# Optimization experiments

Hardware: AMD Instinct MI355X
Metric: run time of the kernel (lower is better)

Reference implementation:

```python
import jax, jax.numpy as jnp
import numpy as np

MIN_DELAY = 60
MAX_DELAY = 420
TAU = 0.0          # module's self.tau (min magnitude for resonant_activation)
TEMPERATURE = 1.0  # forward() default gumbel-softmax temperature


def setup_inputs() -> dict:
    key = jax.random.key(0)
    k1, k2, k3, k4 = jax.random.split(key, 4)
    B, T = 128, 8192
    excitation = jax.random.normal(k1, (B, 1, T), dtype=jnp.float32)
    u = jax.random.uniform(k2, (MAX_DELAY - MIN_DELAY,), dtype=jnp.float32,
                           minval=1e-6, maxval=1.0 - 1e-6)
    gumbel_noise = -jnp.log(-jnp.log(u))  # standard Gumbel samples
    delay_param = jax.random.normal(k3, (MAX_DELAY - MIN_DELAY,), dtype=jnp.float32)
    feedback_gain = jnp.ones((1,), dtype=jnp.float32)
    reflection_coeffs = jax.random.normal(k4, (2,), dtype=jnp.float32)
    return {"excitation": excitation, "gumbel_noise": gumbel_noise,
            "delay_param": delay_param, "feedback_gain": feedback_gain,
            "reflection_coeffs": reflection_coeffs}


def _resonant_activation(x, min_magnitude):
    sign = jnp.sign(x)
    magnitude = jnp.abs(jnp.tanh(x))
    return sign * (min_magnitude + (1.0 - min_magnitude) * magnitude)


def _build_coeffs(gumbel_noise, delay_param, feedback_gain, reflection_coeffs):
    # gumbel_softmax(tau=TEMPERATURE, hard=True) with straight-through estimator
    logits = (delay_param + gumbel_noise) / TEMPERATURE
    soft = jax.nn.softmax(logits)
    hard = jax.nn.one_hot(jnp.argmax(soft), soft.shape[0], dtype=soft.dtype)
    one_hot = jax.lax.stop_gradient(hard - soft) + soft
    shifted = jnp.roll(one_hot, 1)
    # low_pass_bias=False -> tanh, then resonant_activation (applies tanh again, as in source)
    rc = jnp.tanh(reflection_coeffs)
    k1 = _resonant_activation(rc[0], TAU)
    k2 = _resonant_activation(rc[1], TAU)
    a1 = k1 * (1.0 - k2)
    a2 = jnp.clip(k2, -0.999, 0.999)
    a1_bound = 0.999 - jnp.abs(a2)
    a1 = jnp.clip(a1, -a1_bound, a1_bound)
    g = jax.nn.sigmoid(feedback_gain[0]) ** 0.45
    a1 = a1 * g
    a2 = a2 * g
    tail = one_hot * a1 + shifted * a2               # [max_delay - min_delay]
    coeffs = jnp.concatenate([jnp.zeros((MIN_DELAY,), tail.dtype), tail])  # [max_delay]
    return coeffs


def _sample_wise_lpc(x, coeffs):
    # All-pole IIR: y[t] = x[t] - sum_{i=0}^{D-1} coeffs[i] * y[t-1-i]
    B, T = x.shape
    D = coeffs.shape[0]
    buf0 = jnp.zeros((B, D), x.dtype)  # buf[:, i] = y[t-1-i]

    def step(buf, x_t):
        y_t = x_t - buf @ coeffs                              # [B]
        buf = jnp.concatenate([y_t[:, None], buf[:, :-1]], 1)  # shift delay line
        return buf, y_t

    _, ys = jax.lax.scan(step, buf0, x.T)  # ys: [T, B]
    return ys.T


def reference(excitation, gumbel_noise, delay_param, feedback_gain, reflection_coeffs):
    coeffs = _build_coeffs(gumbel_noise, delay_param, feedback_gain, reflection_coeffs)
    x = excitation[:, 0, :]                 # [B, T]
    y = _sample_wise_lpc(x, coeffs)         # [B, T]
    return y[:, None, :]                    # [B, 1, T]
```

## Files before the change

kernel.cpp:

```cpp
#include <hip/hip_runtime.h>
#include <cmath>

#define T_LEN 8192
#define B_ROWS 128
#define ND 360
#define MIN_DELAY_C 60
#define BLOCK 512

__global__ __launch_bounds__(BLOCK) void ks_resonator_kernel(
    const float* __restrict__ excitation,
    const float* __restrict__ gumbel,
    const float* __restrict__ delay_param,
    const float* __restrict__ feedback_gain,
    const float* __restrict__ refl,
    float* __restrict__ out)
{
    __shared__ float y[T_LEN];
    __shared__ float red_v[BLOCK];
    __shared__ int   red_i[BLOCK];
    __shared__ float s_a1, s_a2;
    __shared__ int   s_lagA, s_lagB;

    const int tid = threadIdx.x;
    const int row = blockIdx.x;

    float v = -INFINITY; int idx = 0;
    if (tid < ND) { v = delay_param[tid] + gumbel[tid]; idx = tid; }
    red_v[tid] = v; red_i[tid] = idx;
    __syncthreads();
    for (int off = BLOCK / 2; off > 0; off >>= 1) {
        if (tid < off) {
            float v2 = red_v[tid + off]; int i2 = red_i[tid + off];
            float v1 = red_v[tid];       int i1 = red_i[tid];
            if (v2 > v1 || (v2 == v1 && i2 < i1)) { red_v[tid] = v2; red_i[tid] = i2; }
        }
        __syncthreads();
    }

    if (tid == 0) {
        int p = red_i[0];
        float k1 = tanhf(tanhf(refl[0]));
        float k2 = tanhf(tanhf(refl[1]));
        float a1 = k1 * (1.0f - k2);
        float a2 = fminf(fmaxf(k2, -0.999f), 0.999f);
        float bound = 0.999f - fabsf(a2);
        a1 = fminf(fmaxf(a1, -bound), bound);
        float fg = feedback_gain[0];
        float g = powf(1.0f / (1.0f + expf(-fg)), 0.45f);
        a1 *= g; a2 *= g;
        int p2 = (p + 1) % ND;
        s_a1 = a1; s_a2 = a2;
        s_lagA = MIN_DELAY_C + p + 1;
        s_lagB = MIN_DELAY_C + p2 + 1;
    }
    __syncthreads();

    const float a1 = s_a1, a2 = s_a2;
    const int lagA = s_lagA, lagB = s_lagB;
    const int C = (lagA < lagB) ? lagA : lagB;

    const float* x = excitation + (size_t)row * T_LEN;
    for (int i = tid; i < T_LEN; i += BLOCK) y[i] = x[i];
    __syncthreads();

    for (int pos = 0; pos < T_LEN; pos += C) {
        int end = pos + C; if (end > T_LEN) end = T_LEN;
        for (int j = pos + tid; j < end; j += BLOCK) {
            float ya = (j >= lagA) ? y[j - lagA] : 0.0f;
            float yb = (j >= lagB) ? y[j - lagB] : 0.0f;
            y[j] = y[j] - a1 * ya - a2 * yb;
        }
        __syncthreads();
    }

    float* o = out + (size_t)row * T_LEN;
    for (int i = tid; i < T_LEN; i += BLOCK) o[i] = y[i];
}

extern "C" void kernel_launch(void* const* d_in, const int* in_sizes, int n_in,
                              void* d_out, int out_size, void* d_ws, size_t ws_size,
                              hipStream_t stream) {
    const float* excitation    = (const float*)d_in[0];
    const float* gumbel        = (const float*)d_in[1];
    const float* delay_param   = (const float*)d_in[2];
    const float* feedback_gain = (const float*)d_in[3];
    const float* refl          = (const float*)d_in[4];
    float* out = (float*)d_out;

    ks_resonator_kernel<<<B_ROWS, BLOCK, 0, stream>>>(
        excitation, gumbel, delay_param, feedback_gain, refl, out);
}
```

Before: 73.14 us.

## Run delay-line recurrence in a single wavefront without block barriers

Replaces the block-wide chunked IIR loop, which needed a __syncthreads per chunk, with a single 64-lane wavefront. It processes chunks of 64*K samples, where K is chosen from the smallest lag so each chunk never reads its own outputs. Ordering within the wave relies on in-order LDS access and sched_barrier rather than block barriers. The row load and store are also vectorised to float4, the load is overlapped with the argmax reduction, and the block size is cut to 256. In exchange, the other waves sit idle during the recurrence, and correctness depends on wave-level LDS ordering.

```diff
diff --git a/kernel.cpp b/kernel.cpp
--- a/kernel.cpp
+++ b/kernel.cpp
@@ -5,7 +5,49 @@
 #define B_ROWS 128
 #define ND 360
 #define MIN_DELAY_C 60
-#define BLOCK 512
+#define BLOCK 256
+
+__device__ __forceinline__ void chain_small(float* __restrict__ y, int Wc,
+                                            int lagA, int lagB,
+                                            float a1, float a2, int lane) {
+    for (int pos = 0; pos < T_LEN; pos += Wc) {
+        int end = pos + Wc; if (end > T_LEN) end = T_LEN;
+        int j = pos + lane;
+        if (j < end) {
+            float ya = (j >= lagA) ? y[j - lagA] : 0.0f;
+            float yb = (j >= lagB) ? y[j - lagB] : 0.0f;
+            y[j] = y[j] - a1 * ya - a2 * yb;
+        }
+        __builtin_amdgcn_sched_barrier(0);
+    }
+}
+
+template<int K>
+__device__ __forceinline__ void chain_k(float* __restrict__ y,
+                                        int lagA, int lagB,
+                                        float a1, float a2, int lane) {
+    constexpr int W = 64 * K;
+    for (int pos = 0; pos < T_LEN; pos += W) {
+        float v[K];
+#pragma unroll
+        for (int s = 0; s < K; ++s) {
+            int j = pos + lane + 64 * s;
+            if (j < T_LEN) {
+                float ya = (j >= lagA) ? y[j - lagA] : 0.0f;
+                float yb = (j >= lagB) ? y[j - lagB] : 0.0f;
+                v[s] = y[j] - a1 * ya - a2 * yb;
+            } else {
+                v[s] = 0.0f;
+            }
+        }
+#pragma unroll
+        for (int s = 0; s < K; ++s) {
+            int j = pos + lane + 64 * s;
+            if (j < T_LEN) y[j] = v[s];
+        }
+        __builtin_amdgcn_sched_barrier(0);
+    }
+}
 
 __global__ __launch_bounds__(BLOCK) void ks_resonator_kernel(
     const float* __restrict__ excitation,
@@ -24,8 +66,16 @@
     const int tid = threadIdx.x;
     const int row = blockIdx.x;
 
+    const float4* __restrict__ x4 = (const float4*)(excitation + (size_t)row * T_LEN);
+    float4* y4 = (float4*)y;
+    for (int i = tid; i < T_LEN / 4; i += BLOCK) y4[i] = x4[i];
+
     float v = -INFINITY; int idx = 0;
     if (tid < ND) { v = delay_param[tid] + gumbel[tid]; idx = tid; }
+    if (tid + BLOCK < ND) {
+        float v2 = delay_param[tid + BLOCK] + gumbel[tid + BLOCK];
+        if (v2 > v) { v = v2; idx = tid + BLOCK; }
+    }
     red_v[tid] = v; red_i[tid] = idx;
     __syncthreads();
     for (int off = BLOCK / 2; off > 0; off >>= 1) {
@@ -59,22 +109,25 @@
     const int lagA = s_lagA, lagB = s_lagB;
     const int C = (lagA < lagB) ? lagA : lagB;
 
-    const float* x = excitation + (size_t)row * T_LEN;
-    for (int i = tid; i < T_LEN; i += BLOCK) y[i] = x[i];
+    if (tid < 64) {
+        const int lane = tid;
+        if (C < 64) {
+            chain_small(y, C, lagA, lagB, a1, a2, lane);
+        } else {
+            switch (C >> 6) {
+                case 1:  chain_k<1>(y, lagA, lagB, a1, a2, lane); break;
+                case 2:  chain_k<2>(y, lagA, lagB, a1, a2, lane); break;
+                case 3:  chain_k<3>(y, lagA, lagB, a1, a2, lane); break;
+                case 4:  chain_k<4>(y, lagA, lagB, a1, a2, lane); break;
+                case 5:  chain_k<5>(y, lagA, lagB, a1, a2, lane); break;
+                default: chain_k<6>(y, lagA, lagB, a1, a2, lane); break;
+            }
+        }
+    }
     __syncthreads();
 
-    for (int pos = 0; pos < T_LEN; pos += C) {
-        int end = pos + C; if (end > T_LEN) end = T_LEN;
-        for (int j = pos + tid; j < end; j += BLOCK) {
-            float ya = (j >= lagA) ? y[j - lagA] : 0.0f;
-            float yb = (j >= lagB) ? y[j - lagB] : 0.0f;
-            y[j] = y[j] - a1 * ya - a2 * yb;
-        }
-        __syncthreads();
-    }
-
-    float* o = out + (size_t)row * T_LEN;
-    for (int i = tid; i < T_LEN; i += BLOCK) o[i] = y[i];
+    float4* __restrict__ o4 = (float4*)(out + (size_t)row * T_LEN);
+    for (int i = tid; i < T_LEN / 4; i += BLOCK) o4[i] = y4[i];
 }
 
 extern "C" void kernel_launch(void* const* d_in, const int* in_sizes, int n_in,
```

Result: no change. 72.17 us (-1.3%).

## Factor sparse IIR via cyclic-reduction FIR stages to widen recursion chunks

Applied to the files above, without the earlier changes.

Rewrites the two-tap all-pole recursion with the identity 1/(1+P) = (1-P)(1+P^2)(1+P^4)/(1-P^8), applying three parallel FIR passes whose binomial coefficients are precomputed. After those passes the remaining recursion has lags eight times larger, so the serial chunk width grows eightfold and the number of block-wide barriers drops. It also halves the block size, uses two shared ping-pong buffers, and moves global loads and stores to float4. The higher powers of the coefficients and the extra passes change floating-point rounding order, and the larger shared footprint may lower occupancy.

```diff
diff --git a/kernel.cpp b/kernel.cpp
--- a/kernel.cpp
+++ b/kernel.cpp
@@ -5,7 +5,8 @@
 #define B_ROWS 128
 #define ND 360
 #define MIN_DELAY_C 60
-#define BLOCK 512
+#define BLOCK 256
+
 
 __global__ __launch_bounds__(BLOCK) void ks_resonator_kernel(
     const float* __restrict__ excitation,
@@ -15,17 +16,28 @@
     const float* __restrict__ refl,
     float* __restrict__ out)
 {
-    __shared__ float y[T_LEN];
+    __shared__ float bufA[T_LEN];
+    __shared__ float bufB[T_LEN];
     __shared__ float red_v[BLOCK];
     __shared__ int   red_i[BLOCK];
     __shared__ float s_a1, s_a2;
-    __shared__ int   s_lagA, s_lagB;
+    __shared__ int   s_dA, s_dB;
+    __shared__ float s_c2[3], s_c4[5], s_c8[9];
+    __shared__ int   s_l2[3], s_l4[5], s_l8[9];
 
     const int tid = threadIdx.x;
     const int row = blockIdx.x;
 
+    const float4* __restrict__ x4 = (const float4*)(excitation + (size_t)row * T_LEN);
+    float4* a4 = (float4*)bufA;
+    for (int i = tid; i < T_LEN / 4; i += BLOCK) a4[i] = x4[i];
+
     float v = -INFINITY; int idx = 0;
     if (tid < ND) { v = delay_param[tid] + gumbel[tid]; idx = tid; }
+    if (tid + BLOCK < ND) {
+        float v2 = delay_param[tid + BLOCK] + gumbel[tid + BLOCK];
+        if (v2 > v) { v = v2; idx = tid + BLOCK; }
+    }
     red_v[tid] = v; red_i[tid] = idx;
     __syncthreads();
     for (int off = BLOCK / 2; off > 0; off >>= 1) {
@@ -49,32 +61,85 @@
         float g = powf(1.0f / (1.0f + expf(-fg)), 0.45f);
         a1 *= g; a2 *= g;
         int p2 = (p + 1) % ND;
-        s_a1 = a1; s_a2 = a2;
-        s_lagA = MIN_DELAY_C + p + 1;
-        s_lagB = MIN_DELAY_C + p2 + 1;
+        int dA = MIN_DELAY_C + p + 1;
+        int dB = MIN_DELAY_C + p2 + 1;
+
+        float p1[9], q2[9];
+        p1[0] = 1.0f; q2[0] = 1.0f;
+        for (int i = 1; i < 9; ++i) { p1[i] = p1[i-1] * a1; q2[i] = q2[i-1] * a2; }
+        const float C2[3] = {1.f, 2.f, 1.f};
+        const float C4[5] = {1.f, 4.f, 6.f, 4.f, 1.f};
+        const float C8[9] = {1.f, 8.f, 28.f, 56.f, 70.f, 56.f, 28.f, 8.f, 1.f};
+        for (int i = 0; i < 3; ++i) { s_c2[i] = C2[i] * p1[i] * q2[2-i]; s_l2[i] = i*dA + (2-i)*dB; }
+        for (int i = 0; i < 5; ++i) { s_c4[i] = C4[i] * p1[i] * q2[4-i]; s_l4[i] = i*dA + (4-i)*dB; }
+        for (int i = 0; i < 9; ++i) { s_c8[i] = C8[i] * p1[i] * q2[8-i]; s_l8[i] = i*dA + (8-i)*dB; }
+        s_a1 = a1; s_a2 = a2; s_dA = dA; s_dB = dB;
     }
     __syncthreads();
 
     const float a1 = s_a1, a2 = s_a2;
-    const int lagA = s_lagA, lagB = s_lagB;
-    const int C = (lagA < lagB) ? lagA : lagB;
+    const int dA = s_dA, dB = s_dB;
 
-    const float* x = excitation + (size_t)row * T_LEN;
-    for (int i = tid; i < T_LEN; i += BLOCK) y[i] = x[i];
+    for (int t = tid; t < T_LEN; t += BLOCK) {
+        float acc = bufA[t];
+        if (t >= dA) acc -= a1 * bufA[t - dA];
+        if (t >= dB) acc -= a2 * bufA[t - dB];
+        bufB[t] = acc;
+    }
     __syncthreads();
 
-    for (int pos = 0; pos < T_LEN; pos += C) {
-        int end = pos + C; if (end > T_LEN) end = T_LEN;
-        for (int j = pos + tid; j < end; j += BLOCK) {
-            float ya = (j >= lagA) ? y[j - lagA] : 0.0f;
-            float yb = (j >= lagB) ? y[j - lagB] : 0.0f;
-            y[j] = y[j] - a1 * ya - a2 * yb;
+    {
+        float c0 = s_c2[0], c1 = s_c2[1], c2 = s_c2[2];
+        int   l0 = s_l2[0], l1 = s_l2[1], l2 = s_l2[2];
+        for (int t = tid; t < T_LEN; t += BLOCK) {
+            float acc = bufB[t];
+            if (t >= l0) acc += c0 * bufB[t - l0];
+            if (t >= l1) acc += c1 * bufB[t - l1];
+            if (t >= l2) acc += c2 * bufB[t - l2];
+            bufA[t] = acc;
         }
-        __syncthreads();
+    }
+    __syncthreads();
+
+    {
+        float c[5]; int l[5];
+#pragma unroll
+        for (int k = 0; k < 5; ++k) { c[k] = s_c4[k]; l[k] = s_l4[k]; }
+        for (int t = tid; t < T_LEN; t += BLOCK) {
+            float acc = bufA[t];
+#pragma unroll
+            for (int k = 0; k < 5; ++k) {
+                int s = t - l[k];
+                if (s >= 0) acc += c[k] * bufA[s];
+            }
+            bufB[t] = acc;
+        }
+    }
+    __syncthreads();
+
+    {
+        float c[9]; int l[9];
+#pragma unroll
+        for (int k = 0; k < 9; ++k) { c[k] = s_c8[k]; l[k] = s_l8[k]; }
+        const int W = 8 * (dA < dB ? dA : dB);
+        for (int pos = 0; pos < T_LEN; pos += W) {
+            int end = pos + W; if (end > T_LEN) end = T_LEN;
+            for (int j = pos + tid; j < end; j += BLOCK) {
+                float acc = bufB[j];
+#pragma unroll
+                for (int k = 0; k < 9; ++k) {
+                    int s = j - l[k];
+                    if (s >= 0) acc += c[k] * bufB[s];
+                }
+                bufB[j] = acc;
+            }
+            __syncthreads();
+        }
     }
 
-    float* o = out + (size_t)row * T_LEN;
-    for (int i = tid; i < T_LEN; i += BLOCK) o[i] = y[i];
+    float4* __restrict__ o4 = (float4*)(out + (size_t)row * T_LEN);
+    const float4* b4 = (const float4*)bufB;
+    for (int i = tid; i < T_LEN / 4; i += BLOCK) o4[i] = b4[i];
 }
 
 extern "C" void kernel_launch(void* const* d_in, const int* in_sizes, int n_in,
```

New measurement: 98.24 us. 1.34x slower.
